# Performance work log

Measured on AMD Instinct MI355X. Metric: run time of the kernel, lower is better.

The kernel has to match this reference:

```python
import jax, jax.numpy as jnp
import numpy as np

B, L, D = 1, 2048, 2048
NH, NKV, HD = 32, 8, 64          # heads, kv heads, head_dim = D // NH
THETA = 50000.0
EPS = 1e-5
SCALE = HD ** -0.5


def _rope(x):
    # traditional (interleaved-pair) RoPE; x: (B, H, L, HD)
    hd = x.shape[-1]
    pos = jnp.arange(x.shape[2], dtype=jnp.float32)
    inv = THETA ** (-jnp.arange(0, hd, 2, dtype=jnp.float32) / hd)
    ang = pos[:, None] * inv[None, :]              # (L, HD/2)
    cos, sin = jnp.cos(ang), jnp.sin(ang)
    x1, x2 = x[..., ::2], x[..., 1::2]
    r1 = x1 * cos - x2 * sin
    r2 = x1 * sin + x2 * cos
    return jnp.stack([r1, r2], axis=-1).reshape(x.shape)


def _rmsnorm(x, w):
    return x * jax.lax.rsqrt(jnp.mean(x * x, axis=-1, keepdims=True) + EPS) * w


def setup_inputs() -> dict:
    key = jax.random.key(0)
    ks = jax.random.split(key, 5)
    x = jax.random.normal(ks[0], (B, L, D), dtype=jnp.float32)
    w_qkv = jax.random.normal(ks[1], (NH * HD + 2 * NKV * HD, D), dtype=jnp.float32) * 0.02
    w_out = jax.random.normal(ks[2], (D, D), dtype=jnp.float32) * 0.02
    q_gamma = 1.0 + 0.02 * jax.random.normal(ks[3], (HD,), dtype=jnp.float32)
    k_gamma = 1.0 + 0.02 * jax.random.normal(ks[4], (HD,), dtype=jnp.float32)
    mask = jnp.tril(jnp.ones((L, L), dtype=bool))   # causal
    return {"x": x, "w_qkv": w_qkv, "w_out": w_out,
            "q_gamma": q_gamma, "k_gamma": k_gamma, "mask": mask}


def reference(x, w_qkv, w_out, q_gamma, k_gamma, mask):
    b, l, d = x.shape
    qkv = x @ w_qkv.T                               # fused QKV proj (no bias)
    q, k, v = jnp.split(qkv, [NH * HD, NH * HD + NKV * HD], axis=-1)
    q = q.reshape(b, l, NH, HD).transpose(0, 2, 1, 3)     # (B,NH,L,HD)
    k = k.reshape(b, l, NKV, HD).transpose(0, 2, 1, 3)    # (B,NKV,L,HD)
    v = v.reshape(b, l, NKV, HD).transpose(0, 2, 1, 3)
    q = _rmsnorm(_rope(q), q_gamma)
    k = _rmsnorm(_rope(k), k_gamma)
    g = NH // NKV                                   # GQA group size
    qg = q.reshape(b, NKV, g, l, HD)
    scores = jnp.einsum('bkgqd,bkld->bkgql', qg, k) * SCALE
    scores = jnp.where(mask, scores, -jnp.inf)
    attn = jax.nn.softmax(scores, axis=-1)
    out = jnp.einsum('bkgql,bkld->bkgqd', attn, v)  # (B,NKV,g,L,HD)
    out = out.reshape(b, NH, l, HD).transpose(0, 2, 1, 3).reshape(b, l, d)
    return out @ w_out.T
```

## Files before the change

### kernel.cpp

```cpp
#include <hip/hip_runtime.h>

using bf16   = __bf16;
using bf16x4 = __bf16 __attribute__((ext_vector_type(4)));
using bf16x8 = __bf16 __attribute__((ext_vector_type(8)));
using f32x4  = float __attribute__((ext_vector_type(4)));
using f32x16 = float __attribute__((ext_vector_type(16)));
using u32x2  = unsigned int __attribute__((ext_vector_type(2)));
using u32x4  = unsigned int __attribute__((ext_vector_type(4)));

#define L_SEQ  2048
#define DMODEL 2048
#define NQH    32
#define NKVH   8
#define HDIM   64
#define QKV_N  3072

#define KVF_HSTRIDE (64 * 4 * 64 * 8)

__device__ __forceinline__ void gload_lds16(const void* g, void* lds) {
  __builtin_amdgcn_global_load_lds((__attribute__((address_space(1))) void*)(g),
                                   (__attribute__((address_space(3))) void*)(lds),
                                   16, 0, 0);
}

__device__ __forceinline__ unsigned pack2(float a, float b) {
  union { bf16 h[2]; unsigned u; } x;
  x.h[0] = (bf16)a; x.h[1] = (bf16)b;
  return x.u;
}

__device__ __forceinline__ bf16x8 make_pfrag(float p0, float p1, float p2, float p3,
                                             float p4, float p5, float p6, float p7,
                                             int hi) {
  const unsigned W0 = pack2(p0, p1);
  const unsigned W1 = pack2(p2, p3);
  const unsigned W2 = pack2(p4, p5);
  const unsigned W3 = pack2(p6, p7);
  u32x4 pw;
#if __has_builtin(__builtin_amdgcn_permlane32_swap)
  {
    using i32x2 = int __attribute__((ext_vector_type(2)));
    const i32x2 r02 = __builtin_amdgcn_permlane32_swap((int)W0, (int)W2, false, false);
    const i32x2 r13 = __builtin_amdgcn_permlane32_swap((int)W1, (int)W3, false, false);
    pw = u32x4{ (unsigned)r02[0], (unsigned)r13[0], (unsigned)r02[1], (unsigned)r13[1] };
  }
#else
  {
    const unsigned X0 = (unsigned)__shfl_xor((int)W0, 32);
    const unsigned X1 = (unsigned)__shfl_xor((int)W1, 32);
    const unsigned X2 = (unsigned)__shfl_xor((int)W2, 32);
    const unsigned X3 = (unsigned)__shfl_xor((int)W3, 32);
    pw = u32x4{ hi ? X2 : W0, hi ? X3 : W1, hi ? W2 : X0, hi ? W3 : X1 };
  }
#endif
  return __builtin_bit_cast(bf16x8, pw);
}

__device__ __forceinline__ int chunk_base(int qi) {
  return (qi < 16) ? qi
       : (qi < 32) ? 16 + 2 * (qi - 16)
       : (qi < 48) ? 48 + 3 * (qi - 32)
                   : 96 + 4 * (qi - 48);
}

__global__ void cvt_f32_bf16(const float* __restrict__ in, bf16* __restrict__ out, long n) {
  const long stride = (long)gridDim.x * blockDim.x;
  const long n4 = n >> 2;
  for (long i = (long)blockIdx.x * blockDim.x + threadIdx.x; i < n4; i += stride) {
    const float4 v = reinterpret_cast<const float4*>(in)[i];
    bf16x4 o = { (bf16)v.x, (bf16)v.y, (bf16)v.z, (bf16)v.w };
    reinterpret_cast<bf16x4*>(out)[i] = o;
  }
}

template <typename OutT>
__global__ __launch_bounds__(128)
void gemm_bt(const bf16* __restrict__ A, const bf16* __restrict__ B,
             OutT* __restrict__ C, int M, int N, int K) {
  __shared__ bf16 As[128 * 64];
  __shared__ bf16 Bs[64 * 64];
  const int tid = threadIdx.x;
  const int w = tid >> 6, l = tid & 63;
  const int lq = l & 15, lg = l >> 4;
  const long m0 = (long)blockIdx.y * 128;
  const long n0 = (long)blockIdx.x * 64;

  const int lrow = l >> 3;
  const int scol = ((l & 7) ^ lrow) << 3;

  f32x4 acc[4][4];
#pragma unroll
  for (int i = 0; i < 4; ++i)
#pragma unroll
    for (int j = 0; j < 4; ++j) acc[i][j] = f32x4{0.f, 0.f, 0.f, 0.f};

  for (int k0 = 0; k0 < K; k0 += 64) {
#pragma unroll
    for (int i = 0; i < 8; ++i) {
      const int r0 = (i * 2 + w) * 8;
      gload_lds16(A + (m0 + r0 + lrow) * (long)K + k0 + scol, &As[r0 * 64]);
    }
#pragma unroll
    for (int i = 0; i < 4; ++i) {
      const int r0 = (i * 2 + w) * 8;
      gload_lds16(B + (n0 + r0 + lrow) * (long)K + k0 + scol, &Bs[r0 * 64]);
    }
    __syncthreads();
#pragma unroll
    for (int kk = 0; kk < 2; ++kk) {
      bf16x8 af[4], bfr[4];
#pragma unroll
      for (int t = 0; t < 4; ++t) {
        const int rowA = w * 64 + t * 16 + lq;
        const int blkA = (kk * 4 + lg) ^ (rowA & 7);
        af[t] = *reinterpret_cast<const bf16x8*>(&As[rowA * 64 + blkA * 8]);
        const int rowB = t * 16 + lq;
        const int blkB = (kk * 4 + lg) ^ (rowB & 7);
        bfr[t] = *reinterpret_cast<const bf16x8*>(&Bs[rowB * 64 + blkB * 8]);
      }
#pragma unroll
      for (int mt = 0; mt < 4; ++mt)
#pragma unroll
        for (int nt = 0; nt < 4; ++nt)
          acc[mt][nt] = __builtin_amdgcn_mfma_f32_16x16x32_bf16(af[mt], bfr[nt], acc[mt][nt], 0, 0, 0);
    }
    __syncthreads();
  }

#pragma unroll
  for (int mt = 0; mt < 4; ++mt)
#pragma unroll
    for (int r = 0; r < 4; ++r) {
      const long row = m0 + w * 64 + mt * 16 + lg * 4 + r;
#pragma unroll
      for (int nt = 0; nt < 4; ++nt) {
        const long col = n0 + nt * 16 + lq;
        C[row * (long)N + col] = (OutT)acc[mt][nt][r];
      }
    }
}

__global__ __launch_bounds__(256)
void rope_rms(const bf16* __restrict__ qkv, const float* __restrict__ qg,
              const float* __restrict__ kg, bf16* __restrict__ qo, bf16* __restrict__ kfr) {
  const int gid = blockIdx.x * 4 + (threadIdx.x >> 6);
  const int lane = threadIdx.x & 63;
  const int pos = gid / 40;
  const int hh = gid % 40;
  const bool isq = hh < 32;
  const int col = isq ? hh * HDIM : NQH * HDIM + (hh - 32) * HDIM;

  float x = (float)qkv[(long)pos * QKV_N + col + lane];
  float p = __shfl_xor(x, 1);
  const float fi = (float)(lane & ~1) * (1.0f / 64.0f);
  const float inv = powf(50000.0f, -fi);
  const float ang = (float)pos * inv;
  const float sn = sinf(ang), cs = cosf(ang);
  const float r = (lane & 1) ? (p * sn + x * cs) : (x * cs - p * sn);

  float ss = r * r;
#pragma unroll
  for (int off = 1; off < 64; off <<= 1) ss += __shfl_xor(ss, off);
  const float scl = rsqrtf(ss * (1.0f / 64.0f) + 1e-5f);
  const float g = isq ? qg[lane] : kg[lane];
  const float o = r * scl * g;

  if (isq) {
    qo[(long)pos * DMODEL + hh * HDIM + lane] = (bf16)(o * 0.18033688011112042f);
  } else {
    const int kvh = hh - 32;
    const int d = lane;
    const int lp = (pos & 31) + (((d >> 3) & 1) << 5);
    const long idx = ((((long)kvh * 64 + (pos >> 5)) * 4 + (d >> 4)) * 64 + lp) * 8 + (d & 7);
    kfr[idx] = (bf16)o;
  }
}

__global__ __launch_bounds__(256)
void repack_v(const bf16* __restrict__ qkv, bf16* __restrict__ vfr) {
  __shared__ bf16 t[32][72];
  const int kvh = blockIdx.x >> 6;
  const int kb = blockIdx.x & 63;
  const int tid = threadIdx.x;

  {
    const int row = tid >> 3;
    const int cc = (tid & 7) * 8;
    const bf16* g = qkv + (long)(kb * 32 + row) * QKV_N + (NQH * HDIM + NKVH * HDIM) + kvh * HDIM + cc;
    *reinterpret_cast<u32x4*>(&t[row][cc]) = *reinterpret_cast<const u32x4*>(g);
  }
  __syncthreads();

  const int f = tid >> 6, l = tid & 63;
  const int s = f >> 1, dh = f & 1;
  const int hi = l >> 5, l31 = l & 31;
  union { bf16 b[8]; u32x4 u; } o;
#pragma unroll
  for (int e = 0; e < 8; ++e) o.b[e] = t[s * 16 + hi * 8 + e][dh * 32 + l31];
  bf16* od = vfr + (((long)(kvh * 64 + kb) * 4 + f) * 64 + l) * 8;
  *reinterpret_cast<u32x4*>(od) = o.u;
}

__global__ __launch_bounds__(256)
void flash_attn(const bf16* __restrict__ Q, const bf16* __restrict__ Kfr,
                const bf16* __restrict__ Vfr,
                bf16* __restrict__ po, float* __restrict__ pm, float* __restrict__ pl) {
  const int w = threadIdx.x >> 6, l = threadIdx.x & 63;
  const int lane31 = l & 31, hi = l >> 5;
  const int bb = blockIdx.x;
  const int kvh = bb & 7;
  const int g = bb >> 3;

  int qi, c;
  if (g < 16)      { qi = g;                  c = 0; }
  else if (g < 48) { qi = 16 + ((g - 16) >> 1); c = (g - 16) & 1; }
  else if (g < 96) { qi = 32 + (g - 48) / 3;    c = (g - 48) % 3; }
  else             { qi = 48 + ((g - 96) >> 2); c = (g - 96) & 3; }

  const int h = kvh * 4 + w;
  const int s0 = c * 16;
  const int s1 = min(qi + 1, s0 + 16);
  const int pidx = h * 160 + g;

  const int q0 = qi * 32;
  const int q_abs = q0 + lane31;
  const int l8 = l * 8;

  const bf16* qrow = Q + (long)q_abs * DMODEL + h * HDIM + hi * 8;
  bf16x8 qf[4];
#pragma unroll
  for (int cc = 0; cc < 4; ++cc) qf[cc] = *reinterpret_cast<const bf16x8*>(qrow + cc * 16);

  f32x16 o0, o1;
#pragma unroll
  for (int r = 0; r < 16; ++r) { o0[r] = 0.f; o1[r] = 0.f; }
  float m = -3.0e38f, lsum = 0.f;

  const bf16* kfrh = Kfr + (long)kvh * KVF_HSTRIDE;
  const bf16* vfrh = Vfr + (long)kvh * KVF_HSTRIDE;

  bf16x8 kc0, kc1, kc2, kc3;
  {
    const bf16* kp = kfrh + (long)s0 * 2048 + l8;
    kc0 = *reinterpret_cast<const bf16x8*>(kp);
    kc1 = *reinterpret_cast<const bf16x8*>(kp + 512);
    kc2 = *reinterpret_cast<const bf16x8*>(kp + 1024);
    kc3 = *reinterpret_cast<const bf16x8*>(kp + 1536);
  }

  for (int sti = s0; sti < s1; ++sti) {
    const int kb0 = sti * 32;

    const bf16* vp = vfrh + (long)sti * 2048 + l8;
    const bf16x8 va0 = *reinterpret_cast<const bf16x8*>(vp);
    const bf16x8 vb0 = *reinterpret_cast<const bf16x8*>(vp + 512);
    const bf16x8 va1 = *reinterpret_cast<const bf16x8*>(vp + 1024);
    const bf16x8 vb1 = *reinterpret_cast<const bf16x8*>(vp + 1536);

    const long knoff = (sti + 1 < s1) ? (long)(sti + 1) * 2048 : (long)s0 * 2048;
    const bf16* kp = kfrh + knoff + l8;
    const bf16x8 kn0 = *reinterpret_cast<const bf16x8*>(kp);
    const bf16x8 kn1 = *reinterpret_cast<const bf16x8*>(kp + 512);
    const bf16x8 kn2 = *reinterpret_cast<const bf16x8*>(kp + 1024);
    const bf16x8 kn3 = *reinterpret_cast<const bf16x8*>(kp + 1536);

    f32x16 st;
#pragma unroll
    for (int r = 0; r < 16; ++r) st[r] = 0.f;
    st = __builtin_amdgcn_mfma_f32_32x32x16_bf16(kc0, qf[0], st, 0, 0, 0);
    st = __builtin_amdgcn_mfma_f32_32x32x16_bf16(kc1, qf[1], st, 0, 0, 0);
    st = __builtin_amdgcn_mfma_f32_32x32x16_bf16(kc2, qf[2], st, 0, 0, 0);
    st = __builtin_amdgcn_mfma_f32_32x32x16_bf16(kc3, qf[3], st, 0, 0, 0);

    if (kb0 + 31 > q0) {
#pragma unroll
      for (int r = 0; r < 16; ++r) {
        const int k_abs = kb0 + (r & 3) + 8 * (r >> 2) + 4 * hi;
        if (k_abs > q_abs) st[r] = -3.0e38f;
      }
    }

    float t[8];
#pragma unroll
    for (int r = 0; r < 8; ++r) t[r] = fmaxf(st[r], st[r + 8]);
#pragma unroll
    for (int s = 4; s > 0; s >>= 1)
#pragma unroll
      for (int r = 0; r < 4; ++r) if (r < s) t[r] = fmaxf(t[r], t[r + s]);
    float mx = fmaxf(t[0], __shfl_xor(t[0], 32));

    if (!__all(mx - m <= 8.0f)) {
      const float mn = fmaxf(m, mx);
      const float al = __builtin_amdgcn_exp2f(m - mn);
      m = mn; lsum *= al;
#pragma unroll
      for (int r = 0; r < 16; ++r) { o0[r] *= al; o1[r] *= al; }
    }
    float rs = 0.f;
#pragma unroll
    for (int r = 0; r < 16; ++r) { st[r] = __builtin_amdgcn_exp2f(st[r] - m); rs += st[r]; }
    rs += __shfl_xor(rs, 32);
    lsum += rs;

    {
      const bf16x8 pf0 = make_pfrag(st[0], st[1], st[2], st[3], st[4], st[5], st[6], st[7], hi);
      o0 = __builtin_amdgcn_mfma_f32_32x32x16_bf16(va0, pf0, o0, 0, 0, 0);
      o1 = __builtin_amdgcn_mfma_f32_32x32x16_bf16(vb0, pf0, o1, 0, 0, 0);
      const bf16x8 pf1 = make_pfrag(st[8], st[9], st[10], st[11], st[12], st[13], st[14], st[15], hi);
      o0 = __builtin_amdgcn_mfma_f32_32x32x16_bf16(va1, pf1, o0, 0, 0, 0);
      o1 = __builtin_amdgcn_mfma_f32_32x32x16_bf16(vb1, pf1, o1, 0, 0, 0);
    }

    kc0 = kn0; kc1 = kn1; kc2 = kn2; kc3 = kn3;
  }

  bf16* pbase = po + (long)pidx * 2048 + lane31 * 64;
#pragma unroll
  for (int gg = 0; gg < 4; ++gg) {
    const int d0 = 8 * gg + 4 * hi;
    u32x2 s0v = { pack2(o0[4 * gg + 0], o0[4 * gg + 1]),
                  pack2(o0[4 * gg + 2], o0[4 * gg + 3]) };
    u32x2 s1v = { pack2(o1[4 * gg + 0], o1[4 * gg + 1]),
                  pack2(o1[4 * gg + 2], o1[4 * gg + 3]) };
    *reinterpret_cast<u32x2*>(pbase + d0) = s0v;
    *reinterpret_cast<u32x2*>(pbase + 32 + d0) = s1v;
  }
  if (hi == 0) {
    pm[pidx * 32 + lane31] = m;
    pl[pidx * 32 + lane31] = lsum;
  }
}

__global__ __launch_bounds__(256)
void combine_split(const bf16* __restrict__ po, const float* __restrict__ pm,
                   const float* __restrict__ pl, bf16* __restrict__ ao) {
  const int t = blockIdx.x * 2 + (threadIdx.x >> 7);
  const int tid7 = threadIdx.x & 127;
  const int r = tid7 >> 2;
  const int dc = (tid7 & 3) * 16;
  const int h = t >> 6, qi = t & 63;
  const int nc = 1 + (qi >> 4);
  const int p0 = h * 160 + chunk_base(qi);

  float mv0 = -3e38f, mv1 = -3e38f, mv2 = -3e38f, mv3 = -3e38f;
  float lv0 = 0.f, lv1 = 0.f, lv2 = 0.f, lv3 = 0.f;
  mv0 = pm[(p0 + 0) * 32 + r];              lv0 = pl[(p0 + 0) * 32 + r];
  if (nc > 1) { mv1 = pm[(p0 + 1) * 32 + r]; lv1 = pl[(p0 + 1) * 32 + r]; }
  if (nc > 2) { mv2 = pm[(p0 + 2) * 32 + r]; lv2 = pl[(p0 + 2) * 32 + r]; }
  if (nc > 3) { mv3 = pm[(p0 + 3) * 32 + r]; lv3 = pl[(p0 + 3) * 32 + r]; }
  const float M = fmaxf(fmaxf(mv0, mv1), fmaxf(mv2, mv3));
  const float w0 = __builtin_amdgcn_exp2f(mv0 - M);
  const float w1 = (nc > 1) ? __builtin_amdgcn_exp2f(mv1 - M) : 0.f;
  const float w2 = (nc > 2) ? __builtin_amdgcn_exp2f(mv2 - M) : 0.f;
  const float w3 = (nc > 3) ? __builtin_amdgcn_exp2f(mv3 - M) : 0.f;
  const float invL = 1.0f / (lv0 * w0 + lv1 * w1 + lv2 * w2 + lv3 * w3);

  float acc[16];
#pragma unroll
  for (int j = 0; j < 16; ++j) acc[j] = 0.f;

#pragma unroll
  for (int c = 0; c < 4; ++c) {
    if (c < nc) {
      const float fc = ((c == 0) ? w0 : (c == 1) ? w1 : (c == 2) ? w2 : w3) * invL;
      const bf16* src = po + ((long)(p0 + c) * 2048) + r * 64 + dc;
      const bf16x8 a0 = *reinterpret_cast<const bf16x8*>(src);
      const bf16x8 a1 = *reinterpret_cast<const bf16x8*>(src + 8);
#pragma unroll
      for (int j = 0; j < 8; ++j) {
        acc[j]     += (float)a0[j] * fc;
        acc[8 + j] += (float)a1[j] * fc;
      }
    }
  }

  const long q_abs = (long)qi * 32 + r;
  bf16* od = ao + q_abs * DMODEL + h * HDIM + dc;
  union { bf16 b[16]; u32x4 u[2]; } o;
#pragma unroll
  for (int j = 0; j < 16; ++j) o.b[j] = (bf16)acc[j];
  *reinterpret_cast<u32x4*>(od) = o.u[0];
  *reinterpret_cast<u32x4*>(od + 8) = o.u[1];
}

extern "C" void kernel_launch(void* const* d_in, const int* in_sizes, int n_in,
                              void* d_out, int out_size, void* d_ws, size_t ws_size,
                              hipStream_t stream) {
  const float* x       = (const float*)d_in[0];
  const float* w_qkv   = (const float*)d_in[1];
  const float* w_out   = (const float*)d_in[2];
  const float* q_gamma = (const float*)d_in[3];
  const float* k_gamma = (const float*)d_in[4];

  char* ws = (char*)d_ws;
  bf16* xb  = (bf16*)(ws);
  bf16* wqb = (bf16*)(ws + (8ul  << 20));
  bf16* wob = (bf16*)(ws + (20ul << 20));
  bf16* qkv = (bf16*)(ws + (28ul << 20));
  bf16* qb  = (bf16*)(ws + (40ul << 20));
  bf16* kfr = (bf16*)(ws + (48ul << 20));
  bf16* vfr = (bf16*)(ws + (50ul << 20));
  bf16* ao  = (bf16*)(ws + (52ul << 20));
  bf16*  po = (bf16*)(ws);
  float* pm = (float*)(ws + (28ul << 20));
  float* pl = (float*)(ws + (29ul << 20));
  float* out = (float*)d_out;

  cvt_f32_bf16<<<2048, 256, 0, stream>>>(x, xb, (long)L_SEQ * DMODEL);
  cvt_f32_bf16<<<2048, 256, 0, stream>>>(w_qkv, wqb, (long)QKV_N * DMODEL);
  cvt_f32_bf16<<<2048, 256, 0, stream>>>(w_out, wob, (long)DMODEL * DMODEL);

  gemm_bt<bf16><<<dim3(QKV_N / 64, L_SEQ / 128), 128, 0, stream>>>(xb, wqb, qkv, L_SEQ, QKV_N, DMODEL);

  rope_rms<<<(L_SEQ * 40) / 4, 256, 0, stream>>>(qkv, q_gamma, k_gamma, qb, kfr);
  repack_v<<<NKVH * (L_SEQ / 32), 256, 0, stream>>>(qkv, vfr);

  flash_attn<<<1280, 256, 0, stream>>>(qb, kfr, vfr, po, pm, pl);
  combine_split<<<1024, 256, 0, stream>>>(po, pm, pl, ao);

  gemm_bt<float><<<dim3(DMODEL / 64, L_SEQ / 128), 128, 0, stream>>>(ao, wob, out, L_SEQ, DMODEL, DMODEL);
}
```

Baseline: 172.6 us.

## Split-K the QKV GEMM into two partials and fuse the three conversion kernels

The three fp32-to-bf16 conversion launches are merged into one kernel over the concatenated index range. The QKV projection GEMM gains a split-K grid dimension of 2, writing two bf16 partial outputs that rope_rms and repack_v sum when they load them. The workspace layout is reshuffled so the partial buffers fit. This raises the QKV GEMM's block count (768 to 1536) for better CU occupancy and removes launch overhead, at the cost of extra partial-buffer traffic and an extra bf16 rounding of each partial.

```diff
diff --git a/kernel.cpp b/kernel.cpp
--- a/kernel.cpp
+++ b/kernel.cpp
@@ -63,13 +63,22 @@
                    : 96 + 4 * (qi - 48);
 }
 
-__global__ void cvt_f32_bf16(const float* __restrict__ in, bf16* __restrict__ out, long n) {
+#define N4_X  (L_SEQ * DMODEL / 4)
+#define N4_WQ (QKV_N * DMODEL / 4)
+#define N4_WO (DMODEL * DMODEL / 4)
+__global__ void cvt3_f32_bf16(const float* __restrict__ x, const float* __restrict__ wq,
+                              const float* __restrict__ wo, bf16* __restrict__ xb,
+                              bf16* __restrict__ wqb, bf16* __restrict__ wob) {
   const long stride = (long)gridDim.x * blockDim.x;
-  const long n4 = n >> 2;
-  for (long i = (long)blockIdx.x * blockDim.x + threadIdx.x; i < n4; i += stride) {
-    const float4 v = reinterpret_cast<const float4*>(in)[i];
+  const long ntot = N4_X + N4_WQ + N4_WO;
+  for (long i = (long)blockIdx.x * blockDim.x + threadIdx.x; i < ntot; i += stride) {
+    const float* src; bf16* dst; long j;
+    if (i < N4_X)               { src = x;  dst = xb;  j = i; }
+    else if (i < N4_X + N4_WQ)  { src = wq; dst = wqb; j = i - N4_X; }
+    else                        { src = wo; dst = wob; j = i - N4_X - N4_WQ; }
+    const float4 v = reinterpret_cast<const float4*>(src)[j];
     bf16x4 o = { (bf16)v.x, (bf16)v.y, (bf16)v.z, (bf16)v.w };
-    reinterpret_cast<bf16x4*>(out)[i] = o;
+    reinterpret_cast<bf16x4*>(dst)[j] = o;
   }
 }
 
@@ -84,6 +93,9 @@
   const int lq = l & 15, lg = l >> 4;
   const long m0 = (long)blockIdx.y * 128;
   const long n0 = (long)blockIdx.x * 64;
+  const int ks = K / gridDim.z;
+  const int kb = blockIdx.z * ks;
+  C += (long)blockIdx.z * M * N;
 
   const int lrow = l >> 3;
   const int scol = ((l & 7) ^ lrow) << 3;
@@ -94,7 +106,7 @@
 #pragma unroll
     for (int j = 0; j < 4; ++j) acc[i][j] = f32x4{0.f, 0.f, 0.f, 0.f};
 
-  for (int k0 = 0; k0 < K; k0 += 64) {
+  for (int k0 = kb; k0 < kb + ks; k0 += 64) {
 #pragma unroll
     for (int i = 0; i < 8; ++i) {
       const int r0 = (i * 2 + w) * 8;
@@ -141,8 +153,9 @@
 }
 
 __global__ __launch_bounds__(256)
-void rope_rms(const bf16* __restrict__ qkv, const float* __restrict__ qg,
-              const float* __restrict__ kg, bf16* __restrict__ qo, bf16* __restrict__ kfr) {
+void rope_rms(const bf16* __restrict__ pA, const bf16* __restrict__ pB,
+              const float* __restrict__ qg, const float* __restrict__ kg,
+              bf16* __restrict__ qo, bf16* __restrict__ kfr) {
   const int gid = blockIdx.x * 4 + (threadIdx.x >> 6);
   const int lane = threadIdx.x & 63;
   const int pos = gid / 40;
@@ -150,7 +163,8 @@
   const bool isq = hh < 32;
   const int col = isq ? hh * HDIM : NQH * HDIM + (hh - 32) * HDIM;
 
-  float x = (float)qkv[(long)pos * QKV_N + col + lane];
+  const long idx = (long)pos * QKV_N + col + lane;
+  float x = (float)pA[idx] + (float)pB[idx];
   float p = __shfl_xor(x, 1);
   const float fi = (float)(lane & ~1) * (1.0f / 64.0f);
   const float inv = powf(50000.0f, -fi);
@@ -171,13 +185,14 @@
     const int kvh = hh - 32;
     const int d = lane;
     const int lp = (pos & 31) + (((d >> 3) & 1) << 5);
-    const long idx = ((((long)kvh * 64 + (pos >> 5)) * 4 + (d >> 4)) * 64 + lp) * 8 + (d & 7);
-    kfr[idx] = (bf16)o;
+    const long kidx = ((((long)kvh * 64 + (pos >> 5)) * 4 + (d >> 4)) * 64 + lp) * 8 + (d & 7);
+    kfr[kidx] = (bf16)o;
   }
 }
 
 __global__ __launch_bounds__(256)
-void repack_v(const bf16* __restrict__ qkv, bf16* __restrict__ vfr) {
+void repack_v(const bf16* __restrict__ pA, const bf16* __restrict__ pB,
+              bf16* __restrict__ vfr) {
   __shared__ bf16 t[32][72];
   const int kvh = blockIdx.x >> 6;
   const int kb = blockIdx.x & 63;
@@ -186,8 +201,13 @@
   {
     const int row = tid >> 3;
     const int cc = (tid & 7) * 8;
-    const bf16* g = qkv + (long)(kb * 32 + row) * QKV_N + (NQH * HDIM + NKVH * HDIM) + kvh * HDIM + cc;
-    *reinterpret_cast<u32x4*>(&t[row][cc]) = *reinterpret_cast<const u32x4*>(g);
+    const long goff = (long)(kb * 32 + row) * QKV_N + (NQH * HDIM + NKVH * HDIM) + kvh * HDIM + cc;
+    const bf16x8 a = *reinterpret_cast<const bf16x8*>(pA + goff);
+    const bf16x8 b = *reinterpret_cast<const bf16x8*>(pB + goff);
+    bf16x8 s;
+#pragma unroll
+    for (int e = 0; e < 8; ++e) s[e] = (bf16)((float)a[e] + (float)b[e]);
+    *reinterpret_cast<bf16x8*>(&t[row][cc]) = s;
   }
   __syncthreads();
 
@@ -393,30 +413,29 @@
   const float* k_gamma = (const float*)d_in[4];
 
   char* ws = (char*)d_ws;
-  bf16* xb  = (bf16*)(ws);
-  bf16* wqb = (bf16*)(ws + (8ul  << 20));
-  bf16* wob = (bf16*)(ws + (20ul << 20));
-  bf16* qkv = (bf16*)(ws + (28ul << 20));
-  bf16* qb  = (bf16*)(ws + (40ul << 20));
-  bf16* kfr = (bf16*)(ws + (48ul << 20));
-  bf16* vfr = (bf16*)(ws + (50ul << 20));
-  bf16* ao  = (bf16*)(ws + (52ul << 20));
-  bf16*  po = (bf16*)(ws);
-  float* pm = (float*)(ws + (28ul << 20));
-  float* pl = (float*)(ws + (29ul << 20));
-  float* out = (float*)d_out;
-
-  cvt_f32_bf16<<<2048, 256, 0, stream>>>(x, xb, (long)L_SEQ * DMODEL);
-  cvt_f32_bf16<<<2048, 256, 0, stream>>>(w_qkv, wqb, (long)QKV_N * DMODEL);
-  cvt_f32_bf16<<<2048, 256, 0, stream>>>(w_out, wob, (long)DMODEL * DMODEL);
-
-  gemm_bt<bf16><<<dim3(QKV_N / 64, L_SEQ / 128), 128, 0, stream>>>(xb, wqb, qkv, L_SEQ, QKV_N, DMODEL);
-
-  rope_rms<<<(L_SEQ * 40) / 4, 256, 0, stream>>>(qkv, q_gamma, k_gamma, qb, kfr);
-  repack_v<<<NKVH * (L_SEQ / 32), 256, 0, stream>>>(qkv, vfr);
+  bf16* xb    = (bf16*)(ws);
+  bf16* wqb   = (bf16*)(ws + (8ul  << 20));
+  bf16* wob   = (bf16*)(ws + (20ul << 20));
+  bf16* qkvpA = (bf16*)(ws + (28ul << 20));
+  bf16* qkvpB = (bf16*)(ws + (40ul << 20));
+  bf16* qb    = (bf16*)(ws);
+  bf16* kfr   = (bf16*)(ws + (8ul  << 20));
+  bf16* vfr   = (bf16*)(ws + (10ul << 20));
+  bf16* po    = (bf16*)(ws + (28ul << 20));
+  float* pm   = (float*)(ws + (48ul << 20));
+  float* pl   = (float*)(ws + (49ul << 20));
+  bf16* ao    = (bf16*)(ws + (52ul << 20));
+  float* out  = (float*)d_out;
+
+  cvt3_f32_bf16<<<2048, 256, 0, stream>>>(x, w_qkv, w_out, xb, wqb, wob);
+
+  gemm_bt<bf16><<<dim3(QKV_N / 64, L_SEQ / 128, 2), 128, 0, stream>>>(xb, wqb, qkvpA, L_SEQ, QKV_N, DMODEL);
+
+  rope_rms<<<(L_SEQ * 40) / 4, 256, 0, stream>>>(qkvpA, qkvpB, q_gamma, k_gamma, qb, kfr);
+  repack_v<<<NKVH * (L_SEQ / 32), 256, 0, stream>>>(qkvpA, qkvpB, vfr);
 
   flash_attn<<<1280, 256, 0, stream>>>(qb, kfr, vfr, po, pm, pl);
   combine_split<<<1024, 256, 0, stream>>>(po, pm, pl, ao);
 
-  gemm_bt<float><<<dim3(DMODEL / 64, L_SEQ / 128), 128, 0, stream>>>(ao, wob, out, L_SEQ, DMODEL, DMODEL);
-}
+  gemm_bt<float><<<dim3(DMODEL / 64, L_SEQ / 128, 1), 128, 0, stream>>>(ao, wob, out, L_SEQ, DMODEL, DMODEL);
+}
```

Result: faster. 168.9 us (-2.1%).
